# Kernel tuning notes

Measured on AMD Instinct MI355X. Metric: run time of the kernel, lower is better.

The kernel has to match this reference:

```python
import jax, jax.numpy as jnp
import numpy as np

N = 40000      # nodes
E = 640000     # edges (avg degree 16)
ND = 128       # node_dim
ED = 64        # edge_dim
LN_EPS = 1e-5


def setup_inputs() -> dict:
    key = jax.random.key(0)
    ks = jax.random.split(key, 16)
    s = lambda k, shape, fan_in: jax.random.normal(k, shape, dtype=jnp.float32) * (1.0 / np.sqrt(fan_in))
    return {
        "node_features": jax.random.normal(ks[0], (N, ND), dtype=jnp.float32),
        "edge_indices": jax.random.randint(ks[1], (2, E), 0, N, dtype=jnp.int32),
        "edge_features": jax.random.normal(ks[2], (E, ED), dtype=jnp.float32),
        # message_mlp: Linear(2*ND+ED -> ND), LayerNorm(ND), ReLU, Linear(ND -> ND)
        "W1": s(ks[3], (2 * ND + ED, ND), 2 * ND + ED),
        "b1": jnp.zeros((ND,), jnp.float32),
        "ln_g": jnp.ones((ND,), jnp.float32),
        "ln_b": jnp.zeros((ND,), jnp.float32),
        "W2": s(ks[4], (ND, ND), ND),
        "b2": jnp.zeros((ND,), jnp.float32),
        # edge_gate: Linear(ED -> 1) + Sigmoid
        "gate_w": s(ks[5], (ED, 1), ED),
        "gate_b": jnp.zeros((1,), jnp.float32),
        # GRUCell(ND, ND): weight_ih [3*ND, ND], weight_hh [3*ND, ND] (gates r, z, n)
        "W_ih": s(ks[6], (3 * ND, ND), ND),
        "b_ih": jnp.zeros((3 * ND,), jnp.float32),
        "W_hh": s(ks[7], (3 * ND, ND), ND),
        "b_hh": jnp.zeros((3 * ND,), jnp.float32),
    }


def reference(node_features, edge_indices, edge_features, W1, b1, ln_g, ln_b,
              W2, b2, gate_w, gate_b, W_ih, b_ih, W_hh, b_hh):
    src, dst = edge_indices[0], edge_indices[1]
    # gather src/dst node features and concat with edge features -> [E, 2*ND+ED]
    edge_inputs = jnp.concatenate(
        [node_features[src], node_features[dst], edge_features], axis=1)
    # message MLP: Linear -> LayerNorm -> ReLU -> Linear
    h = edge_inputs @ W1 + b1
    mu = jnp.mean(h, axis=-1, keepdims=True)
    var = jnp.var(h, axis=-1, keepdims=True)
    h = (h - mu) * jax.lax.rsqrt(var + LN_EPS) * ln_g + ln_b
    h = jax.nn.relu(h)
    messages = h @ W2 + b2                                   # [E, ND]
    # sigmoid edge gate from raw edge features
    gate = jax.nn.sigmoid(edge_features @ gate_w + gate_b)   # [E, 1]
    messages = messages * gate
    # scatter-add into destination nodes
    agg = jax.ops.segment_sum(messages, dst, num_segments=node_features.shape[0])
    # GRUCell(input=agg, hidden=node_features), torch gate order: r, z, n
    gi = agg @ W_ih.T + b_ih
    gh = node_features @ W_hh.T + b_hh
    i_r, i_z, i_n = jnp.split(gi, 3, axis=1)
    h_r, h_z, h_n = jnp.split(gh, 3, axis=1)
    r = jax.nn.sigmoid(i_r + h_r)
    z = jax.nn.sigmoid(i_z + h_z)
    n = jnp.tanh(i_n + r * h_n)
    return (1.0 - z) * n + z * node_features
```

## Files before the change

### kernel.cpp

```cpp
#include <hip/hip_runtime.h>
#include <math.h>

#define ND 128
#define ED 64
#define LN_EPS 1e-5f
#define TE 64
#define GSH 136
#define GSF 132

typedef _Float16 f16;
typedef __attribute__((ext_vector_type(8))) _Float16 f16x8;
typedef __attribute__((ext_vector_type(4))) _Float16 f16x4;
typedef __attribute__((ext_vector_type(4))) float f32x4;

__device__ __forceinline__ float sigmoidf_(float x) { return 1.f / (1.f + expf(-x)); }

__global__ void convert_kernel(const float* __restrict__ W1, const float* __restrict__ W2,
                               const float* __restrict__ Wih, const float* __restrict__ Whh,
                               f16* __restrict__ Wcatf, f16* __restrict__ W1ef,
                               f16* __restrict__ W2f,
                               f16* __restrict__ Wihf, f16* __restrict__ Whhf)
{
    int idx = blockIdx.x * 256 + threadIdx.x;
    if (idx < 32768) {
        int cc = idx >> 7, k = idx & 127;
        Wcatf[idx] = (f16)(cc < 128 ? W1[k * 128 + cc] : W1[(128 + k) * 128 + (cc - 128)]);
    } else if (idx < 40960) {
        int i2 = idx - 32768; int n = i2 >> 6, k = i2 & 63;
        W1ef[i2] = (f16)W1[(256 + k) * 128 + n];
    } else if (idx < 57344) {
        int i3 = idx - 40960; int n = i3 >> 7, k = i3 & 127;
        W2f[i3] = (f16)W2[k * 128 + n];
    } else if (idx < 106496) {
        int i4 = idx - 57344;  Wihf[i4] = (f16)Wih[i4];
    } else if (idx < 155648) {
        int i5 = idx - 106496; Whhf[i5] = (f16)Whh[i5];
    }
}

__global__ __launch_bounds__(256)
void h12_kernel(const float* __restrict__ nf, const f16* __restrict__ Wcatf,
                f16* __restrict__ H12f)
{
    __shared__ f16 sa[32 * GSH];
    const int tid  = threadIdx.x;
    const int lane = tid & 63;
    const int w    = __builtin_amdgcn_readfirstlane(tid >> 6);
    const int c    = lane & 15;
    const int quad = lane >> 4;
    const int n0   = blockIdx.x * 32;

    {
        const int r = tid >> 3, q = tid & 7;
        const float* hrow = nf + (size_t)(n0 + r) * ND;
        #pragma unroll
        for (int i = 0; i < 4; ++i) {
            int ec = (q + 8 * i) * 4;
            float4 v = *(const float4*)(hrow + ec);
            f16x4 h; h[0] = (f16)v.x; h[1] = (f16)v.y; h[2] = (f16)v.z; h[3] = (f16)v.w;
            *(f16x4*)(sa + r * GSH + ec) = h;
        }
    }
    __syncthreads();

    f32x4 acc[2][4];
    #pragma unroll
    for (int mt = 0; mt < 2; ++mt)
        #pragma unroll
        for (int nt = 0; nt < 4; ++nt) acc[mt][nt] = (f32x4){0.f, 0.f, 0.f, 0.f};

    #pragma unroll
    for (int ks = 0; ks < 4; ++ks) {
        f16x8 fa[2];
        #pragma unroll
        for (int mt = 0; mt < 2; ++mt)
            fa[mt] = *(const f16x8*)(sa + (16 * mt + c) * GSH + ks * 32 + quad * 8);
        #pragma unroll
        for (int nt = 0; nt < 4; ++nt) {
            f16x8 b = *(const f16x8*)(Wcatf + (64 * w + nt * 16 + c) * 128 + ks * 32 + quad * 8);
            #pragma unroll
            for (int mt = 0; mt < 2; ++mt)
                acc[mt][nt] = __builtin_amdgcn_mfma_f32_16x16x32_f16(fa[mt], b, acc[mt][nt], 0, 0, 0);
        }
    }

    #pragma unroll
    for (int nt = 0; nt < 4; ++nt) {
        int col = 64 * w + nt * 16 + c;
        #pragma unroll
        for (int mt = 0; mt < 2; ++mt)
            #pragma unroll
            for (int r = 0; r < 4; ++r) {
                int row = 16 * mt + 4 * quad + r;
                H12f[(size_t)(n0 + row) * 256 + col] = (f16)acc[mt][nt][r];
            }
    }
}

__global__ void hist_kernel(const int* __restrict__ eidx, int* __restrict__ cnt, int E) {
    int i = blockIdx.x * 256 + threadIdx.x;
    if (i < E) atomicAdd(&cnt[eidx[E + i]], 1);
}

__global__ __launch_bounds__(1024)
void scan_kernel(const int* __restrict__ cnt, int* __restrict__ woff, int N) {
    __shared__ int part[1024];
    const int t = threadIdx.x;
    const int CH = 40;
    int base = t * CH;
    int s = 0;
    for (int i = 0; i < CH; ++i) { int idx = base + i; if (idx < N) s += cnt[idx]; }
    part[t] = s;
    __syncthreads();
    for (int d = 1; d < 1024; d <<= 1) {
        int v = (t >= d) ? part[t - d] : 0;
        __syncthreads();
        part[t] += v;
        __syncthreads();
    }
    int run = (t == 0) ? 0 : part[t - 1];
    for (int i = 0; i < CH; ++i) {
        int idx = base + i;
        if (idx < N) { woff[idx] = run; run += cnt[idx]; }
    }
}

__global__ void scatter_kernel(const int* __restrict__ eidx, int* __restrict__ woff,
                               int* __restrict__ perm, int E) {
    int i = blockIdx.x * 256 + threadIdx.x;
    if (i < E) {
        int p = atomicAdd(&woff[eidx[E + i]], 1);
        perm[p] = i;
    }
}

__global__ __launch_bounds__(256, 4)
void edge_kernel(const f16* __restrict__ H12f, const int* __restrict__ eidx,
                 const float* __restrict__ ef, const int* __restrict__ perm,
                 const f16* __restrict__ W1ef, const float* __restrict__ b1,
                 const float* __restrict__ ln_g, const float* __restrict__ ln_b,
                 const f16* __restrict__ W2f, const float* __restrict__ b2,
                 const float* __restrict__ gate_w, const float* __restrict__ gate_b,
                 float* __restrict__ agg, int E)
{
    __shared__ float smsg[TE * 128];
    __shared__ float sred[TE * 8];
    __shared__ float spart[TE][4];
    __shared__ float sg[TE];
    __shared__ int   se_s[TE], ssrc_s[TE], sdst_s[TE];

    char* shb  = (char*)smsg;
    char* sefb = (char*)smsg + 16384;

    const int tid  = threadIdx.x;
    const int lane = tid & 63;
    const int w    = __builtin_amdgcn_readfirstlane(tid >> 6);
    const int cb   = 32 * w;
    const int c    = lane & 15;
    const int quad = lane >> 4;
    const int e0   = blockIdx.x * TE;

    if (tid < TE) {
        int e = perm[e0 + tid];
        se_s[tid]   = e;
        ssrc_s[tid] = eidx[e];
        sdst_s[tid] = eidx[E + e];
    }
    __syncthreads();

    {
        const int r = tid >> 2, q = tid & 3;
        const f16* h1p = H12f + (size_t)ssrc_s[r] * 256;
        const f16* h2p = H12f + (size_t)sdst_s[r] * 256 + 128;
        const int swz = (r & 7) << 4;
        #pragma unroll
        for (int i = 0; i < 4; ++i) {
            int ch = q + 4 * i;
            f16x8 a = *(const f16x8*)(h1p + ch * 8);
            f16x8 b = *(const f16x8*)(h2p + ch * 8);
            f16x8 s = a + b;
            *(f16x8*)(shb + ((r * 256 + ch * 16) ^ swz)) = s;
        }
        const float* erow = ef + (size_t)se_s[r] * ED;
        float gp = 0.f;
        #pragma unroll
        for (int j = 0; j < 2; ++j) {
            int ch = 2 * q + j;
            const float* p = erow + ch * 8;
            float4 v0 = *(const float4*)p;
            float4 v1 = *(const float4*)(p + 4);
            f16x8 h;
            h[0] = (f16)v0.x; h[1] = (f16)v0.y; h[2] = (f16)v0.z; h[3] = (f16)v0.w;
            h[4] = (f16)v1.x; h[5] = (f16)v1.y; h[6] = (f16)v1.z; h[7] = (f16)v1.w;
            *(f16x8*)(sefb + ((r * 128 + ch * 16) ^ swz)) = h;
            const float* gw = gate_w + ch * 8;
            gp = fmaf(v0.x, gw[0], gp); gp = fmaf(v0.y, gw[1], gp);
            gp = fmaf(v0.z, gw[2], gp); gp = fmaf(v0.w, gw[3], gp);
            gp = fmaf(v1.x, gw[4], gp); gp = fmaf(v1.y, gw[5], gp);
            gp = fmaf(v1.z, gw[6], gp); gp = fmaf(v1.w, gw[7], gp);
        }
        spart[r][q] = gp;
    }
    __syncthreads();

    if (tid < TE)
        sg[tid] = sigmoidf_(spart[tid][0] + spart[tid][1] + spart[tid][2] + spart[tid][3] + gate_b[0]);

    f32x4 acc[4][2];
    #pragma unroll
    for (int mt = 0; mt < 4; ++mt)
        #pragma unroll
        for (int nt = 0; nt < 2; ++nt) acc[mt][nt] = (f32x4){0.f, 0.f, 0.f, 0.f};

    #pragma unroll
    for (int ks = 0; ks < 2; ++ks) {
        f16x8 b0 = *(const f16x8*)(W1ef + (cb + c) * 64 + ks * 32 + quad * 8);
        f16x8 b1v = *(const f16x8*)(W1ef + (cb + 16 + c) * 64 + ks * 32 + quad * 8);
        #pragma unroll
        for (int mt = 0; mt < 4; ++mt) {
            f16x8 a = *(const f16x8*)(sefb + (((16 * mt + c) * 128 + ks * 64 + quad * 16) ^ ((c & 7) << 4)));
            acc[mt][0] = __builtin_amdgcn_mfma_f32_16x16x32_f16(a, b0,  acc[mt][0], 0, 0, 0);
            acc[mt][1] = __builtin_amdgcn_mfma_f32_16x16x32_f16(a, b1v, acc[mt][1], 0, 0, 0);
        }
    }

    float b1c[2], gvc[2], bvc[2], b2c[2];
    #pragma unroll
    for (int nt = 0; nt < 2; ++nt) {
        int col = cb + nt * 16 + c;
        b1c[nt] = b1[col]; gvc[nt] = ln_g[col]; bvc[nt] = ln_b[col]; b2c[nt] = b2[col];
    }
    #pragma unroll
    for (int mt = 0; mt < 4; ++mt) {
        float p1[4] = {0, 0, 0, 0}, p2[4] = {0, 0, 0, 0};
        #pragma unroll
        for (int nt = 0; nt < 2; ++nt)
            #pragma unroll
            for (int r = 0; r < 4; ++r) {
                int row = 16 * mt + 4 * quad + r;
                int col = cb + nt * 16 + c;
                float h12v = (float)(*(const f16*)(shb + ((row * 256 + col * 2) ^ ((row & 7) << 4))));
                float vv = acc[mt][nt][r] + b1c[nt] + h12v;
                acc[mt][nt][r] = vv;
                p1[r] += vv; p2[r] += vv * vv;
            }
        #pragma unroll
        for (int m = 1; m < 16; m <<= 1)
            #pragma unroll
            for (int r = 0; r < 4; ++r) {
                p1[r] += __shfl_xor(p1[r], m);
                p2[r] += __shfl_xor(p2[r], m);
            }
        if (c == 0) {
            #pragma unroll
            for (int r = 0; r < 4; ++r) {
                int row = 16 * mt + 4 * quad + r;
                sred[row * 8 + 2 * w + 0] = p1[r];
                sred[row * 8 + 2 * w + 1] = p2[r];
            }
        }
    }
    __syncthreads();

    #pragma unroll
    for (int mt = 0; mt < 4; ++mt)
        #pragma unroll
        for (int r = 0; r < 4; ++r) {
            int row = 16 * mt + 4 * quad + r;
            f32x4 lo = *(const f32x4*)(sred + row * 8);
            f32x4 hi = *(const f32x4*)(sred + row * 8 + 4);
            float t1 = lo[0] + lo[2] + hi[0] + hi[2];
            float t2 = lo[1] + lo[3] + hi[1] + hi[3];
            float mu = t1 * (1.f / 128.f);
            float var = t2 * (1.f / 128.f) - mu * mu;
            float rs = rsqrtf(var + LN_EPS);
            #pragma unroll
            for (int nt = 0; nt < 2; ++nt) {
                int col = cb + nt * 16 + c;
                float vv = (acc[mt][nt][r] - mu) * rs * gvc[nt] + bvc[nt];
                vv = vv > 0.f ? vv : 0.f;
                *(f16*)(shb + ((row * 256 + col * 2) ^ ((row & 7) << 4))) = (f16)vv;
            }
        }
    __syncthreads();

    f32x4 acc2[4][2];
    #pragma unroll
    for (int mt = 0; mt < 4; ++mt)
        #pragma unroll
        for (int nt = 0; nt < 2; ++nt) acc2[mt][nt] = (f32x4){0.f, 0.f, 0.f, 0.f};
    #pragma unroll
    for (int ks = 0; ks < 4; ++ks) {
        f16x8 b0 = *(const f16x8*)(W2f + (cb + c) * 128 + ks * 32 + quad * 8);
        f16x8 b1v = *(const f16x8*)(W2f + (cb + 16 + c) * 128 + ks * 32 + quad * 8);
        #pragma unroll
        for (int mt = 0; mt < 4; ++mt) {
            f16x8 a = *(const f16x8*)(shb + (((16 * mt + c) * 256 + ks * 64 + quad * 16) ^ ((c & 7) << 4)));
            acc2[mt][0] = __builtin_amdgcn_mfma_f32_16x16x32_f16(a, b0,  acc2[mt][0], 0, 0, 0);
            acc2[mt][1] = __builtin_amdgcn_mfma_f32_16x16x32_f16(a, b1v, acc2[mt][1], 0, 0, 0);
        }
    }
    __syncthreads();

    #pragma unroll
    for (int mt = 0; mt < 4; ++mt)
        #pragma unroll
        for (int r = 0; r < 4; ++r) {
            int row = 16 * mt + 4 * quad + r;
            float gr = sg[row];
            #pragma unroll
            for (int nt = 0; nt < 2; ++nt) {
                int col = cb + nt * 16 + c;
                smsg[(row * 128 + col) ^ ((row & 7) << 2)] = (acc2[mt][nt][r] + b2c[nt]) * gr;
            }
        }
    __syncthreads();

    {
        const int rbase = 16 * w;
        int row0 = rbase;
        float run0 = smsg[(row0 * 128 + lane) ^ ((row0 & 7) << 2)];
        float run1 = smsg[(row0 * 128 + 64 + lane) ^ ((row0 & 7) << 2)];
        int prev = sdst_s[rbase];
        #pragma unroll
        for (int r = 1; r < 16; ++r) {
            int row = rbase + r;
            int d = sdst_s[row];
            float v0 = smsg[(row * 128 + lane) ^ ((row & 7) << 2)];
            float v1 = smsg[(row * 128 + 64 + lane) ^ ((row & 7) << 2)];
            if (d == prev) { run0 += v0; run1 += v1; }
            else {
                atomicAdd(agg + (size_t)prev * ND + lane,      run0);
                atomicAdd(agg + (size_t)prev * ND + 64 + lane, run1);
                run0 = v0; run1 = v1; prev = d;
            }
        }
        atomicAdd(agg + (size_t)prev * ND + lane,      run0);
        atomicAdd(agg + (size_t)prev * ND + 64 + lane, run1);
    }
}

__global__ __launch_bounds__(256, 2)
void gru_kernel(const float* __restrict__ agg, const float* __restrict__ nf,
                const f16* __restrict__ Wihf, const float* __restrict__ b_ih,
                const f16* __restrict__ Whhf, const float* __restrict__ b_hh,
                float* __restrict__ out)
{
    __shared__ f16   sa[32 * GSH];
    __shared__ f16   sh[32 * GSH];
    __shared__ float shf[32 * GSF];

    const int tid  = threadIdx.x;
    const int lane = tid & 63;
    const int w    = __builtin_amdgcn_readfirstlane(tid >> 6);
    const int c    = lane & 15;
    const int quad = lane >> 4;
    const int n0   = blockIdx.x * 32;

    {
        const int r = tid >> 3, q = tid & 7;
        const float* arow = agg + (size_t)(n0 + r) * ND;
        const float* hrow = nf  + (size_t)(n0 + r) * ND;
        #pragma unroll
        for (int i = 0; i < 4; ++i) {
            int ec = (q + 8 * i) * 4;
            float4 va = *(const float4*)(arow + ec);
            f16x4 ha; ha[0] = (f16)va.x; ha[1] = (f16)va.y; ha[2] = (f16)va.z; ha[3] = (f16)va.w;
            *(f16x4*)(sa + r * GSH + ec) = ha;
            float4 vh = *(const float4*)(hrow + ec);
            f16x4 hh; hh[0] = (f16)vh.x; hh[1] = (f16)vh.y; hh[2] = (f16)vh.z; hh[3] = (f16)vh.w;
            *(f16x4*)(sh + r * GSH + ec) = hh;
            *(float4*)(shf + r * GSF + ec) = vh;
        }
    }
    __syncthreads();

    f32x4 aI[2][6], aH[2][6];
    #pragma unroll
    for (int mt = 0; mt < 2; ++mt)
        #pragma unroll
        for (int j = 0; j < 6; ++j) {
            aI[mt][j] = (f32x4){0.f, 0.f, 0.f, 0.f};
            aH[mt][j] = (f32x4){0.f, 0.f, 0.f, 0.f};
        }

    #pragma unroll
    for (int ks = 0; ks < 4; ++ks) {
        f16x8 fa[2], fh[2];
        #pragma unroll
        for (int mt = 0; mt < 2; ++mt) {
            fa[mt] = *(const f16x8*)(sa + (16 * mt + c) * GSH + ks * 32 + quad * 8);
            fh[mt] = *(const f16x8*)(sh + (16 * mt + c) * GSH + ks * 32 + quad * 8);
        }
        #pragma unroll
        for (int gg = 0; gg < 3; ++gg)
            #pragma unroll
            for (int nt = 0; nt < 2; ++nt) {
                int coln = gg * 128 + 32 * w + nt * 16 + c;
                f16x8 bI = *(const f16x8*)(Wihf + coln * 128 + ks * 32 + quad * 8);
                f16x8 bH = *(const f16x8*)(Whhf + coln * 128 + ks * 32 + quad * 8);
                #pragma unroll
                for (int mt = 0; mt < 2; ++mt) {
                    int j = gg * 2 + nt;
                    aI[mt][j] = __builtin_amdgcn_mfma_f32_16x16x32_f16(fa[mt], bI, aI[mt][j], 0, 0, 0);
                    aH[mt][j] = __builtin_amdgcn_mfma_f32_16x16x32_f16(fh[mt], bH, aH[mt][j], 0, 0, 0);
                }
            }
    }

    #pragma unroll
    for (int nt = 0; nt < 2; ++nt) {
        int col = 32 * w + nt * 16 + c;
        float bir = b_ih[col], biz = b_ih[128 + col], bin = b_ih[256 + col];
        float bhr = b_hh[col], bhz = b_hh[128 + col], bhn = b_hh[256 + col];
        #pragma unroll
        for (int mt = 0; mt < 2; ++mt)
            #pragma unroll
            for (int r = 0; r < 4; ++r) {
                int row = 16 * mt + 4 * quad + r;
                float rr = sigmoidf_(aI[mt][0 + nt][r] + bir + aH[mt][0 + nt][r] + bhr);
                float zz = sigmoidf_(aI[mt][2 + nt][r] + biz + aH[mt][2 + nt][r] + bhz);
                float nn = tanhf(aI[mt][4 + nt][r] + bin + rr * (aH[mt][4 + nt][r] + bhn));
                float hp = shf[row * GSF + col];
                out[(size_t)(n0 + row) * ND + col] = (1.f - zz) * nn + zz * hp;
            }
    }
}

extern "C" void kernel_launch(void* const* d_in, const int* in_sizes, int n_in,
                              void* d_out, int out_size, void* d_ws, size_t ws_size,
                              hipStream_t stream) {
    const float* nf     = (const float*)d_in[0];
    const int*   eidx   = (const int*)  d_in[1];
    const float* ef     = (const float*)d_in[2];
    const float* W1     = (const float*)d_in[3];
    const float* b1     = (const float*)d_in[4];
    const float* ln_g   = (const float*)d_in[5];
    const float* ln_b   = (const float*)d_in[6];
    const float* W2     = (const float*)d_in[7];
    const float* b2     = (const float*)d_in[8];
    const float* gate_w = (const float*)d_in[9];
    const float* gate_b = (const float*)d_in[10];
    const float* W_ih   = (const float*)d_in[11];
    const float* b_ih   = (const float*)d_in[12];
    const float* W_hh   = (const float*)d_in[13];
    const float* b_hh   = (const float*)d_in[14];
    float* out = (float*)d_out;

    const int N = in_sizes[0] / ND;
    const int E = in_sizes[1] / 2;

    char* ws = (char*)d_ws;
    float* agg  = (float*)ws;         ws += (size_t)N * ND * 4;
    f16* H12f   = (f16*)ws;           ws += (size_t)N * 256 * 2;
    f16* Wcatf  = (f16*)ws;           ws += 32768 * 2;
    f16* W1ef   = (f16*)ws;           ws += 8192 * 2;
    f16* W2f    = (f16*)ws;           ws += 16384 * 2;
    f16* Wihf   = (f16*)ws;           ws += 49152 * 2;
    f16* Whhf   = (f16*)ws;           ws += 49152 * 2;
    int* cnt    = (int*)ws;           ws += 40960 * 4;
    int* woff   = (int*)ws;           ws += 40960 * 4;
    int* perm   = (int*)ws;           ws += (size_t)E * 4;

    hipMemsetAsync(agg, 0, (size_t)N * ND * 4, stream);
    hipMemsetAsync(cnt, 0, (size_t)N * 4, stream);
    convert_kernel<<<608, 256, 0, stream>>>(W1, W2, W_ih, W_hh,
                                            Wcatf, W1ef, W2f, Wihf, Whhf);
    h12_kernel<<<N / 32, 256, 0, stream>>>(nf, Wcatf, H12f);
    hist_kernel<<<(E + 255) / 256, 256, 0, stream>>>(eidx, cnt, E);
    scan_kernel<<<1, 1024, 0, stream>>>(cnt, woff, N);
    scatter_kernel<<<(E + 255) / 256, 256, 0, stream>>>(eidx, woff, perm, E);
    edge_kernel<<<E / TE, 256, 0, stream>>>(H12f, eidx, ef, perm, W1ef, b1, ln_g, ln_b,
                                            W2f, b2, gate_w, gate_b, agg, E);
    gru_kernel<<<N / 32, 256, 0, stream>>>(agg, nf, Wihf, b_ih, Whhf, b_hh, out);
}
```

Baseline: 562.1 us.

## Fuse small kernels, shrink edge smem to fp16, use fast sigmoid/tanh

Merges weight conversion with the degree histogram, and the perm scatter with the H12 node projection, into single launches. This removes two launches and lets independent work overlap. The edge kernel now keeps its message staging buffer in fp16, which shrinks LDS so occupancy can rise to 5 blocks per CU. It also reduces the gate with wave shuffles, folds bias and H12 into the accumulator init, and raises GRU occupancy. Fast exp and rcp-based sigmoid/tanh replace libm calls, and the fp16 message staging adds rounding error before the atomic accumulation.

```diff
diff --git a/kernel.cpp b/kernel.cpp
--- a/kernel.cpp
+++ b/kernel.cpp
@@ -13,93 +13,42 @@
 typedef __attribute__((ext_vector_type(4))) _Float16 f16x4;
 typedef __attribute__((ext_vector_type(4))) float f32x4;
 
-__device__ __forceinline__ float sigmoidf_(float x) { return 1.f / (1.f + expf(-x)); }
-
-__global__ void convert_kernel(const float* __restrict__ W1, const float* __restrict__ W2,
-                               const float* __restrict__ Wih, const float* __restrict__ Whh,
-                               f16* __restrict__ Wcatf, f16* __restrict__ W1ef,
-                               f16* __restrict__ W2f,
-                               f16* __restrict__ Wihf, f16* __restrict__ Whhf)
+__device__ __forceinline__ float fsigmoid(float x) {
+    return __builtin_amdgcn_rcpf(1.f + __expf(-x));
+}
+__device__ __forceinline__ float ftanh(float x) {
+    return 1.f - 2.f * __builtin_amdgcn_rcpf(1.f + __expf(2.f * x));
+}
+
+__global__ void convert_hist_kernel(const float* __restrict__ W1, const float* __restrict__ W2,
+                                    const float* __restrict__ Wih, const float* __restrict__ Whh,
+                                    const int* __restrict__ eidx,
+                                    f16* __restrict__ Wcatf, f16* __restrict__ W1ef,
+                                    f16* __restrict__ W2f,
+                                    f16* __restrict__ Wihf, f16* __restrict__ Whhf,
+                                    int* __restrict__ cnt, int E)
 {
-    int idx = blockIdx.x * 256 + threadIdx.x;
-    if (idx < 32768) {
-        int cc = idx >> 7, k = idx & 127;
-        Wcatf[idx] = (f16)(cc < 128 ? W1[k * 128 + cc] : W1[(128 + k) * 128 + (cc - 128)]);
-    } else if (idx < 40960) {
-        int i2 = idx - 32768; int n = i2 >> 6, k = i2 & 63;
-        W1ef[i2] = (f16)W1[(256 + k) * 128 + n];
-    } else if (idx < 57344) {
-        int i3 = idx - 40960; int n = i3 >> 7, k = i3 & 127;
-        W2f[i3] = (f16)W2[k * 128 + n];
-    } else if (idx < 106496) {
-        int i4 = idx - 57344;  Wihf[i4] = (f16)Wih[i4];
-    } else if (idx < 155648) {
-        int i5 = idx - 106496; Whhf[i5] = (f16)Whh[i5];
-    }
-}
-
-__global__ __launch_bounds__(256)
-void h12_kernel(const float* __restrict__ nf, const f16* __restrict__ Wcatf,
-                f16* __restrict__ H12f)
-{
-    __shared__ f16 sa[32 * GSH];
-    const int tid  = threadIdx.x;
-    const int lane = tid & 63;
-    const int w    = __builtin_amdgcn_readfirstlane(tid >> 6);
-    const int c    = lane & 15;
-    const int quad = lane >> 4;
-    const int n0   = blockIdx.x * 32;
-
-    {
-        const int r = tid >> 3, q = tid & 7;
-        const float* hrow = nf + (size_t)(n0 + r) * ND;
-        #pragma unroll
-        for (int i = 0; i < 4; ++i) {
-            int ec = (q + 8 * i) * 4;
-            float4 v = *(const float4*)(hrow + ec);
-            f16x4 h; h[0] = (f16)v.x; h[1] = (f16)v.y; h[2] = (f16)v.z; h[3] = (f16)v.w;
-            *(f16x4*)(sa + r * GSH + ec) = h;
-        }
-    }
-    __syncthreads();
-
-    f32x4 acc[2][4];
-    #pragma unroll
-    for (int mt = 0; mt < 2; ++mt)
-        #pragma unroll
-        for (int nt = 0; nt < 4; ++nt) acc[mt][nt] = (f32x4){0.f, 0.f, 0.f, 0.f};
-
-    #pragma unroll
-    for (int ks = 0; ks < 4; ++ks) {
-        f16x8 fa[2];
-        #pragma unroll
-        for (int mt = 0; mt < 2; ++mt)
-            fa[mt] = *(const f16x8*)(sa + (16 * mt + c) * GSH + ks * 32 + quad * 8);
-        #pragma unroll
-        for (int nt = 0; nt < 4; ++nt) {
-            f16x8 b = *(const f16x8*)(Wcatf + (64 * w + nt * 16 + c) * 128 + ks * 32 + quad * 8);
-            #pragma unroll
-            for (int mt = 0; mt < 2; ++mt)
-                acc[mt][nt] = __builtin_amdgcn_mfma_f32_16x16x32_f16(fa[mt], b, acc[mt][nt], 0, 0, 0);
-        }
-    }
-
-    #pragma unroll
-    for (int nt = 0; nt < 4; ++nt) {
-        int col = 64 * w + nt * 16 + c;
-        #pragma unroll
-        for (int mt = 0; mt < 2; ++mt)
-            #pragma unroll
-            for (int r = 0; r < 4; ++r) {
-                int row = 16 * mt + 4 * quad + r;
-                H12f[(size_t)(n0 + row) * 256 + col] = (f16)acc[mt][nt][r];
-            }
-    }
-}
-
-__global__ void hist_kernel(const int* __restrict__ eidx, int* __restrict__ cnt, int E) {
-    int i = blockIdx.x * 256 + threadIdx.x;
-    if (i < E) atomicAdd(&cnt[eidx[E + i]], 1);
+    const int b = blockIdx.x;
+    if (b < 608) {
+        int idx = b * 256 + threadIdx.x;
+        if (idx < 32768) {
+            int cc = idx >> 7, k = idx & 127;
+            Wcatf[idx] = (f16)(cc < 128 ? W1[k * 128 + cc] : W1[(128 + k) * 128 + (cc - 128)]);
+        } else if (idx < 40960) {
+            int i2 = idx - 32768; int n = i2 >> 6, k = i2 & 63;
+            W1ef[i2] = (f16)W1[(256 + k) * 128 + n];
+        } else if (idx < 57344) {
+            int i3 = idx - 40960; int n = i3 >> 7, k = i3 & 127;
+            W2f[i3] = (f16)W2[k * 128 + n];
+        } else if (idx < 106496) {
+            int i4 = idx - 57344;  Wihf[i4] = (f16)Wih[i4];
+        } else if (idx < 155648) {
+            int i5 = idx - 106496; Whhf[i5] = (f16)Whh[i5];
+        }
+    } else {
+        int i = (b - 608) * 256 + threadIdx.x;
+        if (i < E) atomicAdd(&cnt[eidx[E + i]], 1);
+    }
 }
 
 __global__ __launch_bounds__(1024)
@@ -125,16 +74,77 @@
     }
 }
 
-__global__ void scatter_kernel(const int* __restrict__ eidx, int* __restrict__ woff,
-                               int* __restrict__ perm, int E) {
-    int i = blockIdx.x * 256 + threadIdx.x;
-    if (i < E) {
-        int p = atomicAdd(&woff[eidx[E + i]], 1);
-        perm[p] = i;
-    }
-}
-
-__global__ __launch_bounds__(256, 4)
+__global__ __launch_bounds__(256)
+void scatter_h12_kernel(const int* __restrict__ eidx, int* __restrict__ woff,
+                        int* __restrict__ perm, int E, int SB,
+                        const float* __restrict__ nf, const f16* __restrict__ Wcatf,
+                        f16* __restrict__ H12f)
+{
+    __shared__ f16 sa[32 * GSH];
+    const int b = blockIdx.x;
+    if (b < SB) {
+        int i = b * 256 + threadIdx.x;
+        if (i < E) {
+            int p = atomicAdd(&woff[eidx[E + i]], 1);
+            perm[p] = i;
+        }
+        return;
+    }
+    const int tid  = threadIdx.x;
+    const int lane = tid & 63;
+    const int w    = __builtin_amdgcn_readfirstlane(tid >> 6);
+    const int c    = lane & 15;
+    const int quad = lane >> 4;
+    const int n0   = (b - SB) * 32;
+
+    {
+        const int r = tid >> 3, q = tid & 7;
+        const float* hrow = nf + (size_t)(n0 + r) * ND;
+        #pragma unroll
+        for (int i = 0; i < 4; ++i) {
+            int ec = (q + 8 * i) * 4;
+            float4 v = *(const float4*)(hrow + ec);
+            f16x4 h; h[0] = (f16)v.x; h[1] = (f16)v.y; h[2] = (f16)v.z; h[3] = (f16)v.w;
+            *(f16x4*)(sa + r * GSH + ec) = h;
+        }
+    }
+    __syncthreads();
+
+    f32x4 acc[2][4];
+    #pragma unroll
+    for (int mt = 0; mt < 2; ++mt)
+        #pragma unroll
+        for (int nt = 0; nt < 4; ++nt) acc[mt][nt] = (f32x4){0.f, 0.f, 0.f, 0.f};
+
+    #pragma unroll
+    for (int ks = 0; ks < 4; ++ks) {
+        f16x8 fa[2];
+        #pragma unroll
+        for (int mt = 0; mt < 2; ++mt)
+            fa[mt] = *(const f16x8*)(sa + (16 * mt + c) * GSH + ks * 32 + quad * 8);
+        #pragma unroll
+        for (int nt = 0; nt < 4; ++nt) {
+            f16x8 bb = *(const f16x8*)(Wcatf + (64 * w + nt * 16 + c) * 128 + ks * 32 + quad * 8);
+            #pragma unroll
+            for (int mt = 0; mt < 2; ++mt)
+                acc[mt][nt] = __builtin_amdgcn_mfma_f32_16x16x32_f16(fa[mt], bb, acc[mt][nt], 0, 0, 0);
+        }
+    }
+
+    #pragma unroll
+    for (int nt = 0; nt < 4; ++nt) {
+        int col = 64 * w + nt * 16 + c;
+        #pragma unroll
+        for (int mt = 0; mt < 2; ++mt)
+            #pragma unroll
+            for (int r = 0; r < 4; ++r) {
+                int row = 16 * mt + 4 * quad + r;
+                H12f[(size_t)(n0 + row) * 256 + col] = (f16)acc[mt][nt][r];
+            }
+    }
+}
+
+__global__ __launch_bounds__(256, 5)
 void edge_kernel(const f16* __restrict__ H12f, const int* __restrict__ eidx,
                  const float* __restrict__ ef, const int* __restrict__ perm,
                  const f16* __restrict__ W1ef, const float* __restrict__ b1,
@@ -143,14 +153,13 @@
                  const float* __restrict__ gate_w, const float* __restrict__ gate_b,
                  float* __restrict__ agg, int E)
 {
-    __shared__ float smsg[TE * 128];
+    __shared__ f16   smem_h[12288];
     __shared__ float sred[TE * 8];
-    __shared__ float spart[TE][4];
     __shared__ float sg[TE];
     __shared__ int   se_s[TE], ssrc_s[TE], sdst_s[TE];
 
-    char* shb  = (char*)smsg;
-    char* sefb = (char*)smsg + 16384;
+    char* shb  = (char*)smem_h;
+    char* sefb = (char*)smem_h + 16384;
 
     const int tid  = threadIdx.x;
     const int lane = tid & 63;
@@ -199,18 +208,31 @@
             gp = fmaf(v1.x, gw[4], gp); gp = fmaf(v1.y, gw[5], gp);
             gp = fmaf(v1.z, gw[6], gp); gp = fmaf(v1.w, gw[7], gp);
         }
-        spart[r][q] = gp;
-    }
-    __syncthreads();
-
-    if (tid < TE)
-        sg[tid] = sigmoidf_(spart[tid][0] + spart[tid][1] + spart[tid][2] + spart[tid][3] + gate_b[0]);
+        gp += __shfl_xor(gp, 1);
+        gp += __shfl_xor(gp, 2);
+        if (q == 0) sg[r] = fsigmoid(gp + gate_b[0]);
+    }
+    __syncthreads();
+
+    float b1c[2], gvc[2], bvc[2], b2c[2];
+    #pragma unroll
+    for (int nt = 0; nt < 2; ++nt) {
+        int col = cb + nt * 16 + c;
+        b1c[nt] = b1[col]; gvc[nt] = ln_g[col]; bvc[nt] = ln_b[col]; b2c[nt] = b2[col];
+    }
 
     f32x4 acc[4][2];
     #pragma unroll
     for (int mt = 0; mt < 4; ++mt)
         #pragma unroll
-        for (int nt = 0; nt < 2; ++nt) acc[mt][nt] = (f32x4){0.f, 0.f, 0.f, 0.f};
+        for (int nt = 0; nt < 2; ++nt)
+            #pragma unroll
+            for (int r = 0; r < 4; ++r) {
+                int row = 16 * mt + 4 * quad + r;
+                int col = cb + nt * 16 + c;
+                float h12v = (float)(*(const f16*)(shb + ((row * 256 + col * 2) ^ ((row & 7) << 4))));
+                acc[mt][nt][r] = b1c[nt] + h12v;
+            }
 
     #pragma unroll
     for (int ks = 0; ks < 2; ++ks) {
@@ -224,12 +246,6 @@
         }
     }
 
-    float b1c[2], gvc[2], bvc[2], b2c[2];
-    #pragma unroll
-    for (int nt = 0; nt < 2; ++nt) {
-        int col = cb + nt * 16 + c;
-        b1c[nt] = b1[col]; gvc[nt] = ln_g[col]; bvc[nt] = ln_b[col]; b2c[nt] = b2[col];
-    }
     #pragma unroll
     for (int mt = 0; mt < 4; ++mt) {
         float p1[4] = {0, 0, 0, 0}, p2[4] = {0, 0, 0, 0};
@@ -237,11 +253,7 @@
         for (int nt = 0; nt < 2; ++nt)
             #pragma unroll
             for (int r = 0; r < 4; ++r) {
-                int row = 16 * mt + 4 * quad + r;
-                int col = cb + nt * 16 + c;
-                float h12v = (float)(*(const f16*)(shb + ((row * 256 + col * 2) ^ ((row & 7) << 4))));
-                float vv = acc[mt][nt][r] + b1c[nt] + h12v;
-                acc[mt][nt][r] = vv;
+                float vv = acc[mt][nt][r];
                 p1[r] += vv; p2[r] += vv * vv;
             }
         #pragma unroll
@@ -311,7 +323,8 @@
             #pragma unroll
             for (int nt = 0; nt < 2; ++nt) {
                 int col = cb + nt * 16 + c;
-                smsg[(row * 128 + col) ^ ((row & 7) << 2)] = (acc2[mt][nt][r] + b2c[nt]) * gr;
+                *(f16*)(shb + ((row * 256 + col * 2) ^ ((row & 7) << 4))) =
+                    (f16)((acc2[mt][nt][r] + b2c[nt]) * gr);
             }
         }
     __syncthreads();
@@ -319,15 +332,15 @@
     {
         const int rbase = 16 * w;
         int row0 = rbase;
-        float run0 = smsg[(row0 * 128 + lane) ^ ((row0 & 7) << 2)];
-        float run1 = smsg[(row0 * 128 + 64 + lane) ^ ((row0 & 7) << 2)];
+        float run0 = (float)(*(const f16*)(shb + ((row0 * 256 + lane * 2) ^ ((row0 & 7) << 4))));
+        float run1 = (float)(*(const f16*)(shb + ((row0 * 256 + 128 + lane * 2) ^ ((row0 & 7) << 4))));
         int prev = sdst_s[rbase];
         #pragma unroll
         for (int r = 1; r < 16; ++r) {
             int row = rbase + r;
             int d = sdst_s[row];
-            float v0 = smsg[(row * 128 + lane) ^ ((row & 7) << 2)];
-            float v1 = smsg[(row * 128 + 64 + lane) ^ ((row & 7) << 2)];
+            float v0 = (float)(*(const f16*)(shb + ((row * 256 + lane * 2) ^ ((row & 7) << 4))));
+            float v1 = (float)(*(const f16*)(shb + ((row * 256 + 128 + lane * 2) ^ ((row & 7) << 4))));
             if (d == prev) { run0 += v0; run1 += v1; }
             else {
                 atomicAdd(agg + (size_t)prev * ND + lane,      run0);
@@ -340,7 +353,7 @@
     }
 }
 
-__global__ __launch_bounds__(256, 2)
+__global__ __launch_bounds__(256, 3)
 void gru_kernel(const float* __restrict__ agg, const float* __restrict__ nf,
                 const f16* __restrict__ Wihf, const float* __restrict__ b_ih,
                 const f16* __restrict__ Whhf, const float* __restrict__ b_hh,
@@ -418,9 +431,9 @@
             #pragma unroll
             for (int r = 0; r < 4; ++r) {
                 int row = 16 * mt + 4 * quad + r;
-                float rr = sigmoidf_(aI[mt][0 + nt][r] + bir + aH[mt][0 + nt][r] + bhr);
-                float zz = sigmoidf_(aI[mt][2 + nt][r] + biz + aH[mt][2 + nt][r] + bhz);
-                float nn = tanhf(aI[mt][4 + nt][r] + bin + rr * (aH[mt][4 + nt][r] + bhn));
+                float rr = fsigmoid(aI[mt][0 + nt][r] + bir + aH[mt][0 + nt][r] + bhr);
+                float zz = fsigmoid(aI[mt][2 + nt][r] + biz + aH[mt][2 + nt][r] + bhz);
+                float nn = ftanh(aI[mt][4 + nt][r] + bin + rr * (aH[mt][4 + nt][r] + bhn));
                 float hp = shf[row * GSF + col];
                 out[(size_t)(n0 + row) * ND + col] = (1.f - zz) * nn + zz * hp;
             }
@@ -464,12 +477,13 @@
 
     hipMemsetAsync(agg, 0, (size_t)N * ND * 4, stream);
     hipMemsetAsync(cnt, 0, (size_t)N * 4, stream);
-    convert_kernel<<<608, 256, 0, stream>>>(W1, W2, W_ih, W_hh,
-                                            Wcatf, W1ef, W2f, Wihf, Whhf);
-    h12_kernel<<<N / 32, 256, 0, stream>>>(nf, Wcatf, H12f);
-    hist_kernel<<<(E + 255) / 256, 256, 0, stream>>>(eidx, cnt, E);
+
+    const int HB = (E + 255) / 256;
+    convert_hist_kernel<<<608 + HB, 256, 0, stream>>>(
+        W1, W2, W_ih, W_hh, eidx, Wcatf, W1ef, W2f, Wihf, Whhf, cnt, E);
     scan_kernel<<<1, 1024, 0, stream>>>(cnt, woff, N);
-    scatter_kernel<<<(E + 255) / 256, 256, 0, stream>>>(eidx, woff, perm, E);
+    scatter_h12_kernel<<<HB + N / 32, 256, 0, stream>>>(
+        eidx, woff, perm, E, HB, nf, Wcatf, H12f);
     edge_kernel<<<E / TE, 256, 0, stream>>>(H12f, eidx, ef, perm, W1ef, b1, ln_g, ln_b,
                                             W2f, b2, gate_w, gate_b, agg, E);
     gru_kernel<<<N / 32, 256, 0, stream>>>(agg, nf, Wihf, b_ih, Whhf, b_hh, out);
```

New measurement: 624.3 us. 1.11x slower.

## Use fast sigmoid/tanh, shuffle gate reduction, fold bias into accumulators, remap blocks

Applied to the files above, without the earlier changes.

Replaces the expf/tanhf-based sigmoid and tanh with __expf plus hardware reciprocal approximations in both the edge gate and the GRU epilogue. The gate dot-product partials are now reduced with lane shuffles instead of a shared-memory array, which removes one block barrier. The bias and projected node features are preloaded into the MFMA accumulators rather than added afterwards. Edge blocks are remapped with an XCD-style interleave when the grid size is a multiple of 8. These trade a little numerical accuracy and add some index arithmetic in exchange for less math and fewer synchronisations.

```diff
diff --git a/kernel.cpp b/kernel.cpp
--- a/kernel.cpp
+++ b/kernel.cpp
@@ -13,7 +13,12 @@
 typedef __attribute__((ext_vector_type(4))) _Float16 f16x4;
 typedef __attribute__((ext_vector_type(4))) float f32x4;
 
-__device__ __forceinline__ float sigmoidf_(float x) { return 1.f / (1.f + expf(-x)); }
+__device__ __forceinline__ float fsigmoid(float x) {
+    return __builtin_amdgcn_rcpf(1.f + __expf(-x));
+}
+__device__ __forceinline__ float ftanh(float x) {
+    return 1.f - 2.f * __builtin_amdgcn_rcpf(1.f + __expf(2.f * x));
+}
 
 __global__ void convert_kernel(const float* __restrict__ W1, const float* __restrict__ W2,
                                const float* __restrict__ Wih, const float* __restrict__ Whh,
@@ -145,7 +150,6 @@
 {
     __shared__ float smsg[TE * 128];
     __shared__ float sred[TE * 8];
-    __shared__ float spart[TE][4];
     __shared__ float sg[TE];
     __shared__ int   se_s[TE], ssrc_s[TE], sdst_s[TE];
 
@@ -158,7 +162,11 @@
     const int cb   = 32 * w;
     const int c    = lane & 15;
     const int quad = lane >> 4;
-    const int e0   = blockIdx.x * TE;
+
+    const int nwg = gridDim.x;
+    const int bid = blockIdx.x;
+    const int bs  = ((nwg & 7) == 0) ? ((bid & 7) * (nwg >> 3) + (bid >> 3)) : bid;
+    const int e0  = bs * TE;
 
     if (tid < TE) {
         int e = perm[e0 + tid];
@@ -199,18 +207,31 @@
             gp = fmaf(v1.x, gw[4], gp); gp = fmaf(v1.y, gw[5], gp);
             gp = fmaf(v1.z, gw[6], gp); gp = fmaf(v1.w, gw[7], gp);
         }
-        spart[r][q] = gp;
-    }
-    __syncthreads();
-
-    if (tid < TE)
-        sg[tid] = sigmoidf_(spart[tid][0] + spart[tid][1] + spart[tid][2] + spart[tid][3] + gate_b[0]);
+        gp += __shfl_xor(gp, 1);
+        gp += __shfl_xor(gp, 2);
+        if (q == 0) sg[r] = fsigmoid(gp + gate_b[0]);
+    }
+    __syncthreads();
+
+    float b1c[2], gvc[2], bvc[2], b2c[2];
+    #pragma unroll
+    for (int nt = 0; nt < 2; ++nt) {
+        int col = cb + nt * 16 + c;
+        b1c[nt] = b1[col]; gvc[nt] = ln_g[col]; bvc[nt] = ln_b[col]; b2c[nt] = b2[col];
+    }
 
     f32x4 acc[4][2];
     #pragma unroll
     for (int mt = 0; mt < 4; ++mt)
         #pragma unroll
-        for (int nt = 0; nt < 2; ++nt) acc[mt][nt] = (f32x4){0.f, 0.f, 0.f, 0.f};
+        for (int nt = 0; nt < 2; ++nt)
+            #pragma unroll
+            for (int r = 0; r < 4; ++r) {
+                int row = 16 * mt + 4 * quad + r;
+                int col = cb + nt * 16 + c;
+                float h12v = (float)(*(const f16*)(shb + ((row * 256 + col * 2) ^ ((row & 7) << 4))));
+                acc[mt][nt][r] = b1c[nt] + h12v;
+            }
 
     #pragma unroll
     for (int ks = 0; ks < 2; ++ks) {
@@ -224,12 +245,6 @@
         }
     }
 
-    float b1c[2], gvc[2], bvc[2], b2c[2];
-    #pragma unroll
-    for (int nt = 0; nt < 2; ++nt) {
-        int col = cb + nt * 16 + c;
-        b1c[nt] = b1[col]; gvc[nt] = ln_g[col]; bvc[nt] = ln_b[col]; b2c[nt] = b2[col];
-    }
     #pragma unroll
     for (int mt = 0; mt < 4; ++mt) {
         float p1[4] = {0, 0, 0, 0}, p2[4] = {0, 0, 0, 0};
@@ -237,11 +252,7 @@
         for (int nt = 0; nt < 2; ++nt)
             #pragma unroll
             for (int r = 0; r < 4; ++r) {
-                int row = 16 * mt + 4 * quad + r;
-                int col = cb + nt * 16 + c;
-                float h12v = (float)(*(const f16*)(shb + ((row * 256 + col * 2) ^ ((row & 7) << 4))));
-                float vv = acc[mt][nt][r] + b1c[nt] + h12v;
-                acc[mt][nt][r] = vv;
+                float vv = acc[mt][nt][r];
                 p1[r] += vv; p2[r] += vv * vv;
             }
         #pragma unroll
@@ -418,9 +429,9 @@
             #pragma unroll
             for (int r = 0; r < 4; ++r) {
                 int row = 16 * mt + 4 * quad + r;
-                float rr = sigmoidf_(aI[mt][0 + nt][r] + bir + aH[mt][0 + nt][r] + bhr);
-                float zz = sigmoidf_(aI[mt][2 + nt][r] + biz + aH[mt][2 + nt][r] + bhz);
-                float nn = tanhf(aI[mt][4 + nt][r] + bin + rr * (aH[mt][4 + nt][r] + bhn));
+                float rr = fsigmoid(aI[mt][0 + nt][r] + bir + aH[mt][0 + nt][r] + bhr);
+                float zz = fsigmoid(aI[mt][2 + nt][r] + biz + aH[mt][2 + nt][r] + bhz);
+                float nn = ftanh(aI[mt][4 + nt][r] + bin + rr * (aH[mt][4 + nt][r] + bhn));
                 float hp = shf[row * GSF + col];
                 out[(size_t)(n0 + row) * ND + col] = (1.f - zz) * nn + zz * hp;
             }
```

Measured after the change: 581.1 us. 3.4% more time.
